# Kernel optimization log

Measured on AMD Instinct MI355X. Metric: run time of the kernel, lower is better.

## Reference

```python
import jax, jax.numpy as jnp
import numpy as np

BATCH, SEQ, HEADS, EMB = 16, 4096, 16, 64
SHAPE = int(SEQ ** 0.5)          # 64 (2D grid side)
N = 2 * SHAPE - 1                # 127 (circular conv length)


def setup_inputs() -> dict:
    key = jax.random.key(0)
    k_v, k_w = jax.random.split(key)
    v = jax.random.normal(k_v, (BATCH, SEQ, HEADS, EMB), dtype=jnp.float32)
    # 'full' bias base: learned relative bias of length 2*shape_-1 per head
    w = jax.random.normal(k_w, (1, HEADS, N), dtype=jnp.float32)
    o_ = jnp.ones((SHAPE,), dtype=jnp.float32)
    return {"v": v, "w": w, "o_": o_}


def reference(v, w, o_):
    B, S, H, E = v.shape
    s = int(S ** 0.5)
    n = 2 * s - 1

    # bias_base_type == 'full': slice w[..., shape_-s : shape_+s-1] == all of w
    z_fft = jnp.fft.rfft(w)                              # (1, H, n//2+1) complex

    # v: [B, S, H, E] -> [B, E, H, s1, s2]
    vt = jnp.transpose(v, (0, 3, 2, 1)).reshape(B, E, H, s, s)
    v_s = vt.sum(axis=3)                                 # sum over s1 -> [B, E, H, s2]
    u_s = vt.sum(axis=4)                                 # sum over s2 -> [B, E, H, s1]

    pad = ((0, 0), (0, 0), (0, 0), (s - 1, 0))
    v_m_fft = jnp.fft.rfft(jnp.pad(v_s, pad))            # [B, E, H, n//2+1]
    u_m_fft = jnp.fft.rfft(jnp.pad(u_s, pad))

    zf = z_fft[:, None]                                  # (1, 1, H, n//2+1)
    RxV = jnp.fft.irfft(v_m_fft * zf, n=n)[..., :s]      # [B, E, H, s]
    RxU = jnp.fft.irfft(u_m_fft * zf, n=n)[..., :s]      # [B, E, H, s]

    # outer sum over the 2D grid, flatten back to seq
    pbv = RxV[..., None, :] + RxU[..., :, None]          # [B, E, H, s, s]
    pbv = pbv.reshape(B, E, H, S)
    pbv = jnp.transpose(pbv, (0, 3, 2, 1))               # [B, S, H, E]

    # normalizer term z_pb (batch independent)
    o_pad = jnp.pad(o_, ((s - 1, 0),))                   # (n,)
    o_fft = jnp.fft.rfft(o_pad)                          # (n//2+1,)
    z_pb = jnp.fft.irfft(o_fft * z_fft, n=n)[..., :s] * s  # (1, H, s)
    z_pb = z_pb[..., None, :] + z_pb[..., :, None]       # (1, H, s, s)
    z_pb = z_pb.reshape(-1, H, s * s)                    # (1, H, S)
    z_pb = jnp.transpose(z_pb, (0, 2, 1))                # (1, S, H)

    return pbv, z_pb
```

## Files before the change

### kernel.cpp

```cpp
#include <hip/hip_runtime.h>

#define BATCH 16
#define SEQ   4096
#define HEADS 16
#define EMB   64
#define SS    64
#define NW    127

__global__ __launch_bounds__(512) void pbv_kernel(const float* __restrict__ v,
                                                  const float* __restrict__ w,
                                                  float* __restrict__ out) {
    __shared__ float us [SS][SS];
    __shared__ float vsf[SS][SS];
    __shared__ float wtab[NW];

    const int bh   = blockIdx.x;
    const int b    = bh / HEADS;
    const int h    = bh % HEADS;
    const int tid  = threadIdx.x;
    const int wave = tid >> 6;
    const int lane = tid & 63;

    for (int idx = tid; idx < SS * SS; idx += 512) (&vsf[0][0])[idx] = 0.0f;
    if (tid < NW) wtab[tid] = w[h * NW + tid];
    __syncthreads();

    const float* vbase = v + ((size_t)b * SEQ * HEADS + h) * EMB + lane;
    float vsacc[SS];
    #pragma unroll
    for (int j = 0; j < SS; ++j) vsacc[j] = 0.0f;

    for (int ii = 0; ii < 8; ++ii) {
        const int i = wave * 8 + ii;
        const float* rowp = vbase + (size_t)i * SS * (HEADS * EMB);
        float uacc = 0.0f;
        #pragma unroll
        for (int j = 0; j < SS; ++j) {
            float val = rowp[(size_t)j * (HEADS * EMB)];
            uacc += val;
            vsacc[j] += val;
        }
        us[i][lane] = uacc;
    }
    #pragma unroll
    for (int j = 0; j < SS; ++j) atomicAdd(&vsf[j][lane], vsacc[j]);
    __syncthreads();

    float rv[8], ru[8];
    for (int tt = 0; tt < 8; ++tt) {
        const int t = wave * 8 + tt;
        float accv = 0.0f, accu = 0.0f;
        #pragma unroll
        for (int j = 0; j < SS; ++j) {
            int k = t - j + 64;
            if (k >= NW) k -= NW;
            const float c = wtab[k];
            accv += c * vsf[j][lane];
            accu += c * us [j][lane];
        }
        rv[tt] = accv;
        ru[tt] = accu;
    }
    __syncthreads();
    for (int tt = 0; tt < 8; ++tt) {
        const int t = wave * 8 + tt;
        vsf[t][lane] = rv[tt];
        us [t][lane] = ru[tt];
    }
    __syncthreads();

    float* obase = out + ((size_t)b * SEQ * HEADS + h) * EMB + lane;
    for (int ii = 0; ii < 8; ++ii) {
        const int i = wave * 8 + ii;
        const float ruv = us[i][lane];
        #pragma unroll
        for (int j = 0; j < SS; ++j) {
            obase[(size_t)(i * SS + j) * (HEADS * EMB)] = vsf[j][lane] + ruv;
        }
    }
}

__global__ __launch_bounds__(256) void zpb_kernel(const float* __restrict__ w,
                                                  const float* __restrict__ o_,
                                                  float* __restrict__ out2) {
    __shared__ float zp[HEADS][SS];
    __shared__ float osh[SS];
    __shared__ float wsh[HEADS * NW];

    const int tid = threadIdx.x;
    const int g   = blockIdx.x;

    if (tid < SS) osh[tid] = o_[tid];
    for (int idx = tid; idx < HEADS * NW; idx += 256) wsh[idx] = w[idx];
    __syncthreads();

    for (int idx = tid; idx < HEADS * SS; idx += 256) {
        const int h = idx / SS, t = idx % SS;
        float acc = 0.0f;
        #pragma unroll
        for (int j = 0; j < SS; ++j) {
            int k = t - j + 64;
            if (k >= NW) k -= NW;
            acc += osh[j] * wsh[h * NW + k];
        }
        zp[h][t] = acc * (float)SS;
    }
    __syncthreads();

    for (int idx = tid; idx < SS * HEADS; idx += 256) {
        const int tl = idx / HEADS, h = idx % HEADS;
        out2[(size_t)(g * SS + tl) * HEADS + h] = zp[h][tl] + zp[h][g];
    }
}

extern "C" void kernel_launch(void* const* d_in, const int* in_sizes, int n_in,
                              void* d_out, int out_size, void* d_ws, size_t ws_size,
                              hipStream_t stream) {
    const float* v  = (const float*)d_in[0];
    const float* w  = (const float*)d_in[1];
    const float* o_ = (const float*)d_in[2];
    float* out = (float*)d_out;

    pbv_kernel<<<BATCH * HEADS, 512, 0, stream>>>(v, w, out);

    const size_t out1_elems = (size_t)BATCH * SEQ * HEADS * EMB;
    zpb_kernel<<<SS, 256, 0, stream>>>(w, o_, out + out1_elems);
}
```

Before: 482.8 us.

## Split pbv blocks over embedding halves and vectorize loads/stores with float4

Launches twice as many pbv blocks, each covering 32 of the 64 embedding channels. Each thread now handles one grid row and four contiguous channels, reading and writing through float4 accesses. The column sums are accumulated with per-element shared-memory atomics instead of a 64-entry register array. The intent is to raise occupancy and memory-level parallelism on this bandwidth-bound kernel and to cut register pressure, at the cost of many more shared atomics and 128-byte contiguous segments per row.

```diff
diff --git a/kernel.cpp b/kernel.cpp
--- a/kernel.cpp
+++ b/kernel.cpp
@@ -6,77 +6,77 @@
 #define EMB   64
 #define SS    64
 #define NW    127
+#define HE    (HEADS*EMB)
+#define EC    32
 
 __global__ __launch_bounds__(512) void pbv_kernel(const float* __restrict__ v,
                                                   const float* __restrict__ w,
                                                   float* __restrict__ out) {
-    __shared__ float us [SS][SS];
-    __shared__ float vsf[SS][SS];
+    __shared__ float vs_l[SS][EC];
+    __shared__ float us_l[SS][EC];
     __shared__ float wtab[NW];
 
-    const int bh   = blockIdx.x;
-    const int b    = bh / HEADS;
-    const int h    = bh % HEADS;
-    const int tid  = threadIdx.x;
-    const int wave = tid >> 6;
-    const int lane = tid & 63;
+    const int blk   = blockIdx.x;
+    const int bh    = blk >> 1;
+    const int half  = blk & 1;
+    const int b     = bh / HEADS;
+    const int h     = bh % HEADS;
+    const int tid   = threadIdx.x;
+    const int e4    = tid & 7;
+    const int irow  = tid >> 3;
+    const int ebase = half * EC;
 
-    for (int idx = tid; idx < SS * SS; idx += 512) (&vsf[0][0])[idx] = 0.0f;
+    for (int idx = tid; idx < SS * EC; idx += 512) (&vs_l[0][0])[idx] = 0.0f;
     if (tid < NW) wtab[tid] = w[h * NW + tid];
     __syncthreads();
 
-    const float* vbase = v + ((size_t)b * SEQ * HEADS + h) * EMB + lane;
-    float vsacc[SS];
-    #pragma unroll
-    for (int j = 0; j < SS; ++j) vsacc[j] = 0.0f;
-
-    for (int ii = 0; ii < 8; ++ii) {
-        const int i = wave * 8 + ii;
-        const float* rowp = vbase + (size_t)i * SS * (HEADS * EMB);
-        float uacc = 0.0f;
-        #pragma unroll
-        for (int j = 0; j < SS; ++j) {
-            float val = rowp[(size_t)j * (HEADS * EMB)];
-            uacc += val;
-            vsacc[j] += val;
-        }
-        us[i][lane] = uacc;
+    const float* rowbase = v + (((size_t)b * SEQ + (size_t)irow * SS) * HEADS + h) * EMB
+                             + ebase + e4 * 4;
+    float ua = 0.f, ub = 0.f, uc = 0.f, ud = 0.f;
+    #pragma unroll 8
+    for (int j = 0; j < SS; ++j) {
+        const float4 val = *(const float4*)(rowbase + (size_t)j * HE);
+        ua += val.x; ub += val.y; uc += val.z; ud += val.w;
+        atomicAdd(&vs_l[j][e4 * 4 + 0], val.x);
+        atomicAdd(&vs_l[j][e4 * 4 + 1], val.y);
+        atomicAdd(&vs_l[j][e4 * 4 + 2], val.z);
+        atomicAdd(&vs_l[j][e4 * 4 + 3], val.w);
     }
-    #pragma unroll
-    for (int j = 0; j < SS; ++j) atomicAdd(&vsf[j][lane], vsacc[j]);
+    us_l[irow][e4 * 4 + 0] = ua;
+    us_l[irow][e4 * 4 + 1] = ub;
+    us_l[irow][e4 * 4 + 2] = uc;
+    us_l[irow][e4 * 4 + 3] = ud;
     __syncthreads();
 
-    float rv[8], ru[8];
-    for (int tt = 0; tt < 8; ++tt) {
-        const int t = wave * 8 + tt;
-        float accv = 0.0f, accu = 0.0f;
-        #pragma unroll
-        for (int j = 0; j < SS; ++j) {
-            int k = t - j + 64;
-            if (k >= NW) k -= NW;
-            const float c = wtab[k];
-            accv += c * vsf[j][lane];
-            accu += c * us [j][lane];
-        }
-        rv[tt] = accv;
-        ru[tt] = accu;
+    float rva = 0.f, rvb = 0.f, rvc = 0.f, rvd = 0.f;
+    float rua = 0.f, rub = 0.f, ruc = 0.f, rud = 0.f;
+    #pragma unroll 8
+    for (int j = 0; j < SS; ++j) {
+        int k = irow - j + SS;
+        if (k >= NW) k -= NW;
+        const float c = wtab[k];
+        const float4 vv = *(const float4*)&vs_l[j][e4 * 4];
+        const float4 uu = *(const float4*)&us_l[j][e4 * 4];
+        rva += c * vv.x; rvb += c * vv.y; rvc += c * vv.z; rvd += c * vv.w;
+        rua += c * uu.x; rub += c * uu.y; ruc += c * uu.z; rud += c * uu.w;
     }
     __syncthreads();
-    for (int tt = 0; tt < 8; ++tt) {
-        const int t = wave * 8 + tt;
-        vsf[t][lane] = rv[tt];
-        us [t][lane] = ru[tt];
+    {
+        float4 rv; rv.x = rva; rv.y = rvb; rv.z = rvc; rv.w = rvd;
+        float4 ru; ru.x = rua; ru.y = rub; ru.z = ruc; ru.w = rud;
+        *(float4*)&vs_l[irow][e4 * 4] = rv;
+        *(float4*)&us_l[irow][e4 * 4] = ru;
     }
     __syncthreads();
 
-    float* obase = out + ((size_t)b * SEQ * HEADS + h) * EMB + lane;
-    for (int ii = 0; ii < 8; ++ii) {
-        const int i = wave * 8 + ii;
-        const float ruv = us[i][lane];
-        #pragma unroll
-        for (int j = 0; j < SS; ++j) {
-            obase[(size_t)(i * SS + j) * (HEADS * EMB)] = vsf[j][lane] + ruv;
-        }
+    float* obase = out + (((size_t)b * SEQ + (size_t)irow * SS) * HEADS + h) * EMB
+                       + ebase + e4 * 4;
+    const float4 ru = *(const float4*)&us_l[irow][e4 * 4];
+    #pragma unroll 8
+    for (int j = 0; j < SS; ++j) {
+        float4 o = *(const float4*)&vs_l[j][e4 * 4];
+        o.x += ru.x; o.y += ru.y; o.z += ru.z; o.w += ru.w;
+        *(float4*)(obase + (size_t)j * HE) = o;
     }
 }
 
@@ -121,7 +121,7 @@
     const float* o_ = (const float*)d_in[2];
     float* out = (float*)d_out;
 
-    pbv_kernel<<<BATCH * HEADS, 512, 0, stream>>>(v, w, out);
+    pbv_kernel<<<BATCH * HEADS * 2, 512, 0, stream>>>(v, w, out);
 
     const size_t out1_elems = (size_t)BATCH * SEQ * HEADS * EMB;
     zpb_kernel<<<SS, 256, 0, stream>>>(w, o_, out + out1_elems);
```

After: 737.0 us. 52.7% more time.
